# Kernel tuning notes

Measured on AMD Instinct MI355X. Metric: run time of the kernel, lower is better.

## Reference

```python
import jax, jax.numpy as jnp
import numpy as np

HIST_LEN = 100  # STDP history cap in the original module


def setup_inputs() -> dict:
    key = jax.random.key(0)
    ks = jax.random.split(key, 5)
    H, B = 1024, 16384
    return {
        "x": jax.random.normal(ks[0], (B, H), dtype=jnp.float32),
        "weights": jax.random.normal(ks[1], (H, H), dtype=jnp.float32) * 0.1,
        "meta_plasticity": jnp.ones((H,), dtype=jnp.float32),
        "pre_hist": jax.random.normal(ks[2], (HIST_LEN, H), dtype=jnp.float32) * 0.1,
        "post_hist": jax.random.normal(ks[3], (HIST_LEN, H), dtype=jnp.float32) * 0.1,
        "activity_history": jnp.zeros((1000,), dtype=jnp.float32),
        "history_pointer": 5,
        "stdp_window": jnp.float32(20.0),
        "stdp_decay": jnp.float32(0.1),
        "target_activity": jnp.float32(0.1),
        "homeostatic_rate": jnp.float32(0.01),
        "meta_learning_rate": jnp.float32(0.001),
    }


def reference(x, weights, meta_plasticity, pre_hist, post_hist,
              activity_history, history_pointer, stdp_window, stdp_decay,
              target_activity, homeostatic_rate, meta_learning_rate):
    # --- forward matmul: weights * meta_plasticity scales columns (broadcast over rows)
    output = x @ (weights * meta_plasticity)  # [B, H]

    # --- STDP update (vectorized form of the python loop over the history) ---
    # append current mean activities, pop oldest (steady-state length == HIST_LEN)
    pre = jnp.concatenate([pre_hist[1:], x.mean(axis=0)[None]], axis=0)       # [L, H]
    post = jnp.concatenate([post_hist[1:], output.mean(axis=0)[None]], axis=0)
    L = HIST_LEN
    i = jnp.arange(L, dtype=jnp.float32)
    dt = (L - i) * stdp_window
    w = 0.01 * jnp.exp(-dt * stdp_decay)                                      # [L]
    pos_w = jnp.where(i < L - 1, w, 0.0)   # i < len-1 branch
    neg_w = jnp.where(i > 0, w, 0.0)       # i > 0 branch
    # sum_i pos_w[i] * outer(post[-1], pre[i]) = outer(post[-1], pos_w @ pre)
    dW = jnp.outer(post[-1], pos_w @ pre) - jnp.outer(neg_w @ post, pre[-1])
    new_w = jnp.clip(weights + dW, -1.0, 1.0)

    # --- homeostatic plasticity ---
    hist = activity_history.at[history_pointer].set(output.mean())
    activity_diff = target_activity - hist.mean()
    new_w = jnp.clip(new_w * (1.0 + homeostatic_rate * activity_diff), -1.0, 1.0)

    # --- meta plasticity ---
    new_meta = jnp.clip(
        meta_plasticity + meta_learning_rate * (output.mean(axis=0) - meta_plasticity),
        0.0, 2.0)

    return output, new_w, new_meta, hist
```

## Files before the change

### kernel.cpp

```cpp
#include <hip/hip_runtime.h>
#include <hip/hip_bf16.h>

#define H 1024
#define BATCH 16384

typedef unsigned short u16;
typedef u16 u16x8 __attribute__((ext_vector_type(8)));
typedef __bf16 bf16x8 __attribute__((ext_vector_type(8)));
typedef float f32x4 __attribute__((ext_vector_type(4)));

typedef __attribute__((address_space(3))) unsigned int lds_uint;
typedef __attribute__((address_space(1))) const unsigned int glob_uint;

__device__ __forceinline__ u16 f2bf(float f) {
  unsigned int u = __float_as_uint(f);
  u += 0x7fffu + ((u >> 16) & 1u);
  return (u16)(u >> 16);
}

__global__ __launch_bounds__(256) void convx_kernel(const float* __restrict__ X,
                                                    u16* __restrict__ Xb,
                                                    float* __restrict__ xsum) {
  size_t r0 = (size_t)blockIdx.x * 64;
  int c = threadIdx.x;
  float s0 = 0.f, s1 = 0.f, s2 = 0.f, s3 = 0.f;
#pragma unroll 4
  for (int r = 0; r < 64; ++r) {
    size_t off = (r0 + r) * H + c * 4;
    const float4 v = *(const float4*)&X[off];
    ushort4 h;
    h.x = f2bf(v.x); h.y = f2bf(v.y); h.z = f2bf(v.z); h.w = f2bf(v.w);
    *(ushort4*)&Xb[off] = h;
    s0 += v.x; s1 += v.y; s2 += v.z; s3 += v.w;
  }
  atomicAdd(&xsum[c * 4 + 0], s0);
  atomicAdd(&xsum[c * 4 + 1], s1);
  atomicAdd(&xsum[c * 4 + 2], s2);
  atomicAdd(&xsum[c * 4 + 3], s3);
}

__global__ __launch_bounds__(256) void convw_kernel(const float* __restrict__ W,
                                                    u16* __restrict__ Wbt) {
  __shared__ __align__(16) u16 t[64][72];
  const int tid = threadIdx.x;
  const int n0 = blockIdx.x * 64, k0 = blockIdx.y * 64;
  const int rb = tid >> 4, c4 = tid & 15;
#pragma unroll
  for (int i = 0; i < 4; ++i) {
    int r = rb + i * 16;
    const float4 v = *(const float4*)&W[(size_t)(k0 + r) * H + n0 + c4 * 4];
    t[c4 * 4 + 0][r] = f2bf(v.x);
    t[c4 * 4 + 1][r] = f2bf(v.y);
    t[c4 * 4 + 2][r] = f2bf(v.z);
    t[c4 * 4 + 3][r] = f2bf(v.w);
  }
  __syncthreads();
  const int seg = tid & 7;
#pragma unroll
  for (int p = 0; p < 2; ++p) {
    int wr = p * 32 + (tid >> 3);
    *(u16x8*)&Wbt[(size_t)(n0 + wr) * H + k0 + seg * 8] = *(const u16x8*)&t[wr][seg * 8];
  }
}

__global__ __launch_bounds__(256) void gemm2_kernel(const u16* __restrict__ Xb,
                                                    const u16* __restrict__ Wbt,
                                                    const float* __restrict__ meta,
                                                    float* __restrict__ out) {
  __shared__ __align__(16) u16 lA[128 * 32];
  __shared__ __align__(16) u16 lB[128 * 32];

  const int tid = threadIdx.x;
  const int wave = tid >> 6;
  const int lane = tid & 63;
  const int quad = lane >> 4;
  const int l16 = lane & 15;
  const int wm = wave >> 1, wn = wave & 1;
  const size_t row0 = (size_t)blockIdx.x * 128;
  const int col0 = blockIdx.y * 128;

  const int sr = lane >> 2;
  const int sk = (lane & 3) * 8;

  f32x4 acc[4][4];
#pragma unroll
  for (int i = 0; i < 4; ++i)
#pragma unroll
    for (int j = 0; j < 4; ++j) acc[i][j] = (f32x4){0.f, 0.f, 0.f, 0.f};

  for (int k0 = 0; k0 < H; k0 += 32) {
#pragma unroll
    for (int i = 0; i < 2; ++i) {
      const int rg = i * 64 + wave * 16;
      const u16* ga = &Xb[(row0 + rg + sr) * H + k0 + sk];
      const u16* gb = &Wbt[(size_t)(col0 + rg + sr) * H + k0 + sk];
      __builtin_amdgcn_global_load_lds((glob_uint*)ga, (lds_uint*)&lA[rg * 32], 16, 0, 0);
      __builtin_amdgcn_global_load_lds((glob_uint*)gb, (lds_uint*)&lB[rg * 32], 16, 0, 0);
    }
    __syncthreads();

    bf16x8 av[4], bv[4];
#pragma unroll
    for (int f = 0; f < 4; ++f) {
      av[f] = __builtin_bit_cast(bf16x8, *(const u16x8*)&lA[(wm * 64 + f * 16 + l16) * 32 + quad * 8]);
      bv[f] = __builtin_bit_cast(bf16x8, *(const u16x8*)&lB[(wn * 64 + f * 16 + l16) * 32 + quad * 8]);
    }
#pragma unroll
    for (int fm = 0; fm < 4; ++fm)
#pragma unroll
      for (int fn = 0; fn < 4; ++fn)
        acc[fm][fn] = __builtin_amdgcn_mfma_f32_16x16x32_bf16(av[fm], bv[fn], acc[fm][fn], 0, 0, 0);
    __syncthreads();
  }

  float mcol[4];
#pragma unroll
  for (int fn = 0; fn < 4; ++fn) mcol[fn] = meta[col0 + wn * 64 + fn * 16 + l16];
#pragma unroll
  for (int fm = 0; fm < 4; ++fm) {
#pragma unroll
    for (int fn = 0; fn < 4; ++fn) {
      int col = col0 + wn * 64 + fn * 16 + l16;
#pragma unroll
      for (int r = 0; r < 4; ++r) {
        size_t row = row0 + wm * 64 + fm * 16 + quad * 4 + r;
        out[row * H + col] = acc[fm][fn][r] * mcol[fn];
      }
    }
  }
}

__global__ __launch_bounds__(256) void colsum_kernel(const float* __restrict__ x,
                                                     float* __restrict__ xsum) {
  int col = blockIdx.x * 256 + threadIdx.x;
  size_t r0 = (size_t)blockIdx.y * 256;
  float s = 0.f;
#pragma unroll 8
  for (int r = 0; r < 256; ++r) s += x[(r0 + r) * H + col];
  atomicAdd(&xsum[col], s);
}

__global__ __launch_bounds__(256) void gemm_fallback_kernel(const float* __restrict__ X,
                                                            const float* __restrict__ W,
                                                            const float* __restrict__ meta,
                                                            float* __restrict__ out) {
  __shared__ __align__(16) u16 lA[128][40];
  __shared__ __align__(16) u16 lB[128][40];
  const int tid = threadIdx.x;
  const int wave = tid >> 6;
  const int lane = tid & 63;
  const int quad = lane >> 4;
  const int l16 = lane & 15;
  const int wm = wave >> 1, wn = wave & 1;
  const size_t row0 = (size_t)blockIdx.x * 128;
  const int col0 = blockIdx.y * 128;
  f32x4 acc[4][4];
#pragma unroll
  for (int i = 0; i < 4; ++i)
#pragma unroll
    for (int j = 0; j < 4; ++j) acc[i][j] = (f32x4){0.f, 0.f, 0.f, 0.f};
  for (int k0 = 0; k0 < H; k0 += 32) {
#pragma unroll
    for (int i = 0; i < 4; ++i) {
      int idx = i * 256 + tid;
      int r = idx >> 3, c4 = idx & 7;
      const float4 v = *(const float4*)&X[(row0 + r) * H + k0 + c4 * 4];
      ushort4 h;
      h.x = f2bf(v.x); h.y = f2bf(v.y); h.z = f2bf(v.z); h.w = f2bf(v.w);
      *(ushort4*)&lA[r][c4 * 4] = h;
    }
#pragma unroll
    for (int i = 0; i < 4; ++i) {
      int idx = i * 256 + tid;
      int kk = idx >> 5, c4 = idx & 31;
      const float4 v = *(const float4*)&W[(size_t)(k0 + kk) * H + col0 + c4 * 4];
      lB[c4 * 4 + 0][kk] = f2bf(v.x);
      lB[c4 * 4 + 1][kk] = f2bf(v.y);
      lB[c4 * 4 + 2][kk] = f2bf(v.z);
      lB[c4 * 4 + 3][kk] = f2bf(v.w);
    }
    __syncthreads();
    bf16x8 av[4], bv[4];
#pragma unroll
    for (int f = 0; f < 4; ++f) {
      av[f] = __builtin_bit_cast(bf16x8, *(const u16x8*)&lA[wm * 64 + f * 16 + l16][quad * 8]);
      bv[f] = __builtin_bit_cast(bf16x8, *(const u16x8*)&lB[wn * 64 + f * 16 + l16][quad * 8]);
    }
#pragma unroll
    for (int fm = 0; fm < 4; ++fm)
#pragma unroll
      for (int fn = 0; fn < 4; ++fn)
        acc[fm][fn] = __builtin_amdgcn_mfma_f32_16x16x32_bf16(av[fm], bv[fn], acc[fm][fn], 0, 0, 0);
    __syncthreads();
  }
  float mcol[4];
#pragma unroll
  for (int fn = 0; fn < 4; ++fn) mcol[fn] = meta[col0 + wn * 64 + fn * 16 + l16];
#pragma unroll
  for (int fm = 0; fm < 4; ++fm) {
#pragma unroll
    for (int fn = 0; fn < 4; ++fn) {
      int col = col0 + wn * 64 + fn * 16 + l16;
#pragma unroll
      for (int r = 0; r < 4; ++r) {
        size_t row = row0 + wm * 64 + fm * 16 + quad * 4 + r;
        out[row * H + col] = acc[fm][fn][r] * mcol[fn];
      }
    }
  }
}

__global__ __launch_bounds__(256) void vecmat_kernel(const float* __restrict__ W,
                                                     const float* __restrict__ xsum,
                                                     float* __restrict__ outraw) {
  int j = blockIdx.x * 256 + threadIdx.x;
  int k0 = blockIdx.y * 64;
  float s = 0.f;
#pragma unroll 8
  for (int k = 0; k < 64; ++k) s += xsum[k0 + k] * W[(size_t)(k0 + k) * H + j];
  atomicAdd(&outraw[j], s * (1.0f / (float)BATCH));
}

__global__ __launch_bounds__(256) void stdpvec_kernel(const float* __restrict__ pre,
                                                      const float* __restrict__ post,
                                                      const float* __restrict__ win,
                                                      const float* __restrict__ dec,
                                                      float* __restrict__ posv,
                                                      float* __restrict__ negh) {
  int col = blockIdx.x * 256 + threadIdx.x;
  int t0 = 1 + blockIdx.y * 20;
  float wd = win[0] * dec[0];
  float ps = 0.f, ns = 0.f;
  int tend = t0 + 20;
  if (tend > 100) tend = 100;
  for (int t = t0; t < tend; ++t) {
    float w = 0.01f * expf(-(float)(101 - t) * wd);
    ps += w * pre[t * H + col];
    if (t >= 2) ns += w * post[t * H + col];
  }
  atomicAdd(&posv[col], ps);
  atomicAdd(&negh[col], ns);
}

__global__ __launch_bounds__(1024) void finalize_kernel(const float* __restrict__ meta,
                                                        const float* __restrict__ act,
                                                        const int* __restrict__ ptr,
                                                        const float* __restrict__ targ,
                                                        const float* __restrict__ homeo,
                                                        const float* __restrict__ mlr,
                                                        const float* __restrict__ outraw,
                                                        float* __restrict__ outmean,
                                                        float* __restrict__ scalep,
                                                        float* __restrict__ meta_out,
                                                        float* __restrict__ hist_out) {
  __shared__ float r1[16], r2[16];
  __shared__ float sc[2];
  int t = threadIdx.x;
  float om = meta[t] * outraw[t];
  outmean[t] = om;
  float a = (t < 1000) ? act[t] : 0.f;
  float s1 = om, s2 = a;
#pragma unroll
  for (int o = 32; o > 0; o >>= 1) {
    s1 += __shfl_down(s1, o, 64);
    s2 += __shfl_down(s2, o, 64);
  }
  if ((t & 63) == 0) { r1[t >> 6] = s1; r2[t >> 6] = s2; }
  __syncthreads();
  if (t == 0) {
    float ts1 = 0.f, ts2 = 0.f;
#pragma unroll
    for (int i = 0; i < 16; ++i) { ts1 += r1[i]; ts2 += r2[i]; }
    float total_mean = ts1 / (float)H;
    int p = ptr[0];
    float hist_mean = (ts2 - act[p] + total_mean) / 1000.f;
    float diff = targ[0] - hist_mean;
    sc[0] = 1.f + homeo[0] * diff;
    sc[1] = total_mean;
    scalep[0] = sc[0];
  }
  __syncthreads();
  float nm = meta[t] + mlr[0] * (om - meta[t]);
  nm = fminf(fmaxf(nm, 0.f), 2.f);
  meta_out[t] = nm;
  if (t < 1000) hist_out[t] = (t == ptr[0]) ? sc[1] : act[t];
}

__global__ __launch_bounds__(256) void neww_kernel(const float* __restrict__ W,
                                                   const float* __restrict__ outmean,
                                                   const float* __restrict__ posv,
                                                   const float* __restrict__ negh,
                                                   const float* __restrict__ xsum,
                                                   const float* __restrict__ scalep,
                                                   const float* __restrict__ win,
                                                   const float* __restrict__ dec,
                                                   float* __restrict__ out) {
  int idx = blockIdx.x * 256 + threadIdx.x;
  int rr = idx >> 10;
  int cc = idx & 1023;
  float w99 = 0.01f * expf(-win[0] * dec[0]);
  float scale = scalep[0];
  float om_r = outmean[rr];
  float neg_r = negh[rr] + w99 * om_r;
  float v = W[idx] + om_r * posv[cc] - neg_r * (xsum[cc] * (1.0f / (float)BATCH));
  v = fminf(fmaxf(v, -1.f), 1.f);
  v = v * scale;
  v = fminf(fmaxf(v, -1.f), 1.f);
  out[idx] = v;
}

extern "C" void kernel_launch(void* const* d_in, const int* in_sizes, int n_in,
                              void* d_out, int out_size, void* d_ws, size_t ws_size,
                              hipStream_t stream) {
  const float* x     = (const float*)d_in[0];
  const float* W     = (const float*)d_in[1];
  const float* meta  = (const float*)d_in[2];
  const float* pre   = (const float*)d_in[3];
  const float* post  = (const float*)d_in[4];
  const float* act   = (const float*)d_in[5];
  const int*   ptr   = (const int*)d_in[6];
  const float* win   = (const float*)d_in[7];
  const float* dec   = (const float*)d_in[8];
  const float* targ  = (const float*)d_in[9];
  const float* homeo = (const float*)d_in[10];
  const float* mlr   = (const float*)d_in[11];

  float* out_y    = (float*)d_out;
  float* out_w    = out_y + (size_t)BATCH * H;
  float* out_meta = out_w + (size_t)H * H;
  float* out_hist = out_meta + H;

  float* ws      = (float*)d_ws;
  float* xsum    = ws;
  float* outraw  = ws + 1024;
  float* outmean = ws + 2048;
  float* posv    = ws + 3072;
  float* negh    = ws + 4096;
  float* scalep  = ws + 5120;
  u16* Xb  = (u16*)(ws + 6144);
  u16* Wbt = Xb + (size_t)BATCH * H;

  const size_t ws_need = 6144 * sizeof(float) + ((size_t)BATCH * H + (size_t)H * H) * sizeof(u16);

  hipMemsetAsync(d_ws, 0, 6144 * sizeof(float), stream);

  if (ws_size >= ws_need) {
    convx_kernel<<<256, 256, 0, stream>>>(x, Xb, xsum);
    convw_kernel<<<dim3(16, 16), 256, 0, stream>>>(W, Wbt);
    gemm2_kernel<<<dim3(128, 8), 256, 0, stream>>>(Xb, Wbt, meta, out_y);
  } else {
    colsum_kernel<<<dim3(4, 64), 256, 0, stream>>>(x, xsum);
    gemm_fallback_kernel<<<dim3(128, 8), 256, 0, stream>>>(x, W, meta, out_y);
  }
  vecmat_kernel<<<dim3(4, 16), 256, 0, stream>>>(W, xsum, outraw);
  stdpvec_kernel<<<dim3(4, 5), 256, 0, stream>>>(pre, post, win, dec, posv, negh);
  finalize_kernel<<<1, 1024, 0, stream>>>(meta, act, ptr, targ, homeo, mlr,
                                          outraw, outmean, scalep, out_meta, out_hist);
  neww_kernel<<<4096, 256, 0, stream>>>(W, outmean, posv, negh, xsum, scalep, win, dec, out_w);
}
```

Measured before the change: 242.2 us.

## Merge prep, vecmat and STDP kernels; deepen GEMM K-tile; vectorize weight update

Merges the X conversion, W transpose-conversion and STDP vector partial sums into one launch that writes per-block partial column sums instead of using atomics, which removes the workspace memset. The vector-matrix product for output means now runs as extra blocks inside the GEMM launch. The GEMM K step doubles to 64 so each loop iteration has one barrier pair per 64 columns instead of per 32. The final weight update uses float4 loads and stores. Together this cuts launch count and serialization between small kernels, at the cost of a larger workspace and an extra reduction pass over the partial sums.

```diff
diff --git a/kernel.cpp b/kernel.cpp
--- a/kernel.cpp
+++ b/kernel.cpp
@@ -18,69 +18,121 @@
   return (u16)(u >> 16);
 }
 
-__global__ __launch_bounds__(256) void convx_kernel(const float* __restrict__ X,
-                                                    u16* __restrict__ Xb,
-                                                    float* __restrict__ xsum) {
-  size_t r0 = (size_t)blockIdx.x * 64;
-  int c = threadIdx.x;
-  float s0 = 0.f, s1 = 0.f, s2 = 0.f, s3 = 0.f;
+#define WS_XSUMP   0
+#define WS_XSUM    (WS_XSUMP + 256 * H)
+#define WS_ORAWP   (WS_XSUM + H)
+#define WS_POSVP   (WS_ORAWP + 16 * H)
+#define WS_NEGHP   (WS_POSVP + 5 * H)
+#define WS_OUTMEAN (WS_NEGHP + 5 * H)
+#define WS_POSV    (WS_OUTMEAN + H)
+#define WS_NEGH    (WS_POSV + H)
+#define WS_SCALEP  (WS_NEGH + H)
+#define WS_BF16    (WS_SCALEP + 16)
+
+__global__ __launch_bounds__(256) void prep_kernel(const float* __restrict__ X,
+                                                   const float* __restrict__ W,
+                                                   u16* __restrict__ Xb,
+                                                   u16* __restrict__ Wbt,
+                                                   float* __restrict__ ws,
+                                                   const float* __restrict__ pre,
+                                                   const float* __restrict__ post,
+                                                   const float* __restrict__ win,
+                                                   const float* __restrict__ dec) {
+  __shared__ __align__(16) u16 t[64][72];
+  const int b = blockIdx.x, tid = threadIdx.x;
+  if (b < 256) {
+    size_t r0 = (size_t)b * 64;
+    float s0 = 0.f, s1 = 0.f, s2 = 0.f, s3 = 0.f;
 #pragma unroll 4
-  for (int r = 0; r < 64; ++r) {
-    size_t off = (r0 + r) * H + c * 4;
-    const float4 v = *(const float4*)&X[off];
-    ushort4 h;
-    h.x = f2bf(v.x); h.y = f2bf(v.y); h.z = f2bf(v.z); h.w = f2bf(v.w);
-    *(ushort4*)&Xb[off] = h;
-    s0 += v.x; s1 += v.y; s2 += v.z; s3 += v.w;
-  }
-  atomicAdd(&xsum[c * 4 + 0], s0);
-  atomicAdd(&xsum[c * 4 + 1], s1);
-  atomicAdd(&xsum[c * 4 + 2], s2);
-  atomicAdd(&xsum[c * 4 + 3], s3);
-}
-
-__global__ __launch_bounds__(256) void convw_kernel(const float* __restrict__ W,
-                                                    u16* __restrict__ Wbt) {
-  __shared__ __align__(16) u16 t[64][72];
-  const int tid = threadIdx.x;
-  const int n0 = blockIdx.x * 64, k0 = blockIdx.y * 64;
-  const int rb = tid >> 4, c4 = tid & 15;
-#pragma unroll
-  for (int i = 0; i < 4; ++i) {
-    int r = rb + i * 16;
-    const float4 v = *(const float4*)&W[(size_t)(k0 + r) * H + n0 + c4 * 4];
-    t[c4 * 4 + 0][r] = f2bf(v.x);
-    t[c4 * 4 + 1][r] = f2bf(v.y);
-    t[c4 * 4 + 2][r] = f2bf(v.z);
-    t[c4 * 4 + 3][r] = f2bf(v.w);
-  }
-  __syncthreads();
-  const int seg = tid & 7;
-#pragma unroll
-  for (int p = 0; p < 2; ++p) {
-    int wr = p * 32 + (tid >> 3);
-    *(u16x8*)&Wbt[(size_t)(n0 + wr) * H + k0 + seg * 8] = *(const u16x8*)&t[wr][seg * 8];
-  }
-}
-
-__global__ __launch_bounds__(256) void gemm2_kernel(const u16* __restrict__ Xb,
-                                                    const u16* __restrict__ Wbt,
-                                                    const float* __restrict__ meta,
-                                                    float* __restrict__ out) {
-  __shared__ __align__(16) u16 lA[128 * 32];
-  __shared__ __align__(16) u16 lB[128 * 32];
-
-  const int tid = threadIdx.x;
+    for (int r = 0; r < 64; ++r) {
+      size_t off = (r0 + r) * H + tid * 4;
+      const float4 v = *(const float4*)&X[off];
+      ushort4 h;
+      h.x = f2bf(v.x); h.y = f2bf(v.y); h.z = f2bf(v.z); h.w = f2bf(v.w);
+      *(ushort4*)&Xb[off] = h;
+      s0 += v.x; s1 += v.y; s2 += v.z; s3 += v.w;
+    }
+    float* row = &ws[WS_XSUMP + b * H];
+    row[tid * 4 + 0] = s0; row[tid * 4 + 1] = s1;
+    row[tid * 4 + 2] = s2; row[tid * 4 + 3] = s3;
+  } else if (b < 512) {
+    const int b2 = b - 256;
+    const int n0 = (b2 & 15) * 64, k0 = (b2 >> 4) * 64;
+    const int rb = tid >> 4, c4 = tid & 15;
+#pragma unroll
+    for (int i = 0; i < 4; ++i) {
+      int r = rb + i * 16;
+      const float4 v = *(const float4*)&W[(size_t)(k0 + r) * H + n0 + c4 * 4];
+      t[c4 * 4 + 0][r] = f2bf(v.x);
+      t[c4 * 4 + 1][r] = f2bf(v.y);
+      t[c4 * 4 + 2][r] = f2bf(v.z);
+      t[c4 * 4 + 3][r] = f2bf(v.w);
+    }
+    __syncthreads();
+    const int seg = tid & 7;
+#pragma unroll
+    for (int p = 0; p < 2; ++p) {
+      int wr = p * 32 + (tid >> 3);
+      *(u16x8*)&Wbt[(size_t)(n0 + wr) * H + k0 + seg * 8] = *(const u16x8*)&t[wr][seg * 8];
+    }
+  } else {
+    const int b2 = b - 512;
+    const int col = (b2 & 3) * 256 + tid;
+    const int seg = b2 >> 2;
+    const int t0 = 1 + seg * 20;
+    int tend = t0 + 20; if (tend > 100) tend = 100;
+    float wd = win[0] * dec[0];
+    float ps = 0.f, ns = 0.f;
+    for (int tt = t0; tt < tend; ++tt) {
+      float w = 0.01f * expf(-(float)(101 - tt) * wd);
+      ps += w * pre[tt * H + col];
+      if (tt >= 2) ns += w * post[tt * H + col];
+    }
+    ws[WS_POSVP + seg * H + col] = ps;
+    ws[WS_NEGHP + seg * H + col] = ns;
+  }
+}
+
+__global__ __launch_bounds__(256) void gemm_vm_kernel(const u16* __restrict__ Xb,
+                                                      const u16* __restrict__ Wbt,
+                                                      const float* __restrict__ meta,
+                                                      const float* __restrict__ W,
+                                                      float* __restrict__ ws,
+                                                      float* __restrict__ out) {
+  __shared__ __align__(16) u16 lA[8192];
+  __shared__ __align__(16) u16 lB[8192];
+  __shared__ float xs[64];
+
+  const int b = blockIdx.x, tid = threadIdx.x;
+
+  if (b < 64) {
+    const int jx = b & 3, ky = b >> 2;
+    if (tid < 64) {
+      float s = 0.f;
+      const float* p = &ws[WS_XSUMP + ky * 64 + tid];
+#pragma unroll 8
+      for (int q = 0; q < 256; ++q) s += p[q * H];
+      xs[tid] = s;
+      if (jx == 0) ws[WS_XSUM + ky * 64 + tid] = s;
+    }
+    __syncthreads();
+    const int j = jx * 256 + tid;
+    float s = 0.f;
+#pragma unroll 8
+    for (int k = 0; k < 64; ++k) s += xs[k] * W[(size_t)(ky * 64 + k) * H + j];
+    ws[WS_ORAWP + ky * H + j] = s * (1.0f / (float)BATCH);
+    return;
+  }
+
+  const int bg = b - 64;
+  const int mt = bg & 127, nt = bg >> 7;
+  const size_t row0 = (size_t)mt * 128;
+  const int col0 = nt * 128;
   const int wave = tid >> 6;
   const int lane = tid & 63;
   const int quad = lane >> 4;
   const int l16 = lane & 15;
   const int wm = wave >> 1, wn = wave & 1;
-  const size_t row0 = (size_t)blockIdx.x * 128;
-  const int col0 = blockIdx.y * 128;
-
-  const int sr = lane >> 2;
-  const int sk = (lane & 3) * 8;
 
   f32x4 acc[4][4];
 #pragma unroll
@@ -88,28 +140,37 @@
 #pragma unroll
     for (int j = 0; j < 4; ++j) acc[i][j] = (f32x4){0.f, 0.f, 0.f, 0.f};
 
-  for (int k0 = 0; k0 < H; k0 += 32) {
-#pragma unroll
-    for (int i = 0; i < 2; ++i) {
-      const int rg = i * 64 + wave * 16;
-      const u16* ga = &Xb[(row0 + rg + sr) * H + k0 + sk];
-      const u16* gb = &Wbt[(size_t)(col0 + rg + sr) * H + k0 + sk];
-      __builtin_amdgcn_global_load_lds((glob_uint*)ga, (lds_uint*)&lA[rg * 32], 16, 0, 0);
-      __builtin_amdgcn_global_load_lds((glob_uint*)gb, (lds_uint*)&lB[rg * 32], 16, 0, 0);
-    }
-    __syncthreads();
-
-    bf16x8 av[4], bv[4];
-#pragma unroll
-    for (int f = 0; f < 4; ++f) {
-      av[f] = __builtin_bit_cast(bf16x8, *(const u16x8*)&lA[(wm * 64 + f * 16 + l16) * 32 + quad * 8]);
-      bv[f] = __builtin_bit_cast(bf16x8, *(const u16x8*)&lB[(wn * 64 + f * 16 + l16) * 32 + quad * 8]);
-    }
-#pragma unroll
-    for (int fm = 0; fm < 4; ++fm)
-#pragma unroll
-      for (int fn = 0; fn < 4; ++fn)
-        acc[fm][fn] = __builtin_amdgcn_mfma_f32_16x16x32_bf16(av[fm], bv[fn], acc[fm][fn], 0, 0, 0);
+  for (int k0 = 0; k0 < H; k0 += 64) {
+#pragma unroll
+    for (int i = 0; i < 4; ++i) {
+      const int c = wave * 4 + i;
+      const int half = c >> 3;
+      const int rr = (c & 7) * 16 + (lane >> 2);
+      const int kk = half * 32 + (lane & 3) * 8;
+      const u16* ga = &Xb[(row0 + rr) * H + k0 + kk];
+      const u16* gb = &Wbt[(size_t)(col0 + rr) * H + k0 + kk];
+      u16* la = &lA[half * 4096 + (c & 7) * 512];
+      u16* lb = &lB[half * 4096 + (c & 7) * 512];
+      __builtin_amdgcn_global_load_lds((glob_uint*)ga, (lds_uint*)la, 16, 0, 0);
+      __builtin_amdgcn_global_load_lds((glob_uint*)gb, (lds_uint*)lb, 16, 0, 0);
+    }
+    __syncthreads();
+#pragma unroll
+    for (int ks = 0; ks < 2; ++ks) {
+      bf16x8 av[4], bv[4];
+#pragma unroll
+      for (int f = 0; f < 4; ++f) {
+        av[f] = __builtin_bit_cast(bf16x8,
+            *(const u16x8*)&lA[ks * 4096 + (wm * 64 + f * 16 + l16) * 32 + quad * 8]);
+        bv[f] = __builtin_bit_cast(bf16x8,
+            *(const u16x8*)&lB[ks * 4096 + (wn * 64 + f * 16 + l16) * 32 + quad * 8]);
+      }
+#pragma unroll
+      for (int fm = 0; fm < 4; ++fm)
+#pragma unroll
+        for (int fn = 0; fn < 4; ++fn)
+          acc[fm][fn] = __builtin_amdgcn_mfma_f32_16x16x32_bf16(av[fm], bv[fn], acc[fm][fn], 0, 0, 0);
+    }
     __syncthreads();
   }
 
@@ -128,6 +189,92 @@
       }
     }
   }
+}
+
+__global__ __launch_bounds__(1024) void finalize2_kernel(const float* __restrict__ meta,
+                                                         const float* __restrict__ act,
+                                                         const int* __restrict__ ptr,
+                                                         const float* __restrict__ targ,
+                                                         const float* __restrict__ homeo,
+                                                         const float* __restrict__ mlr,
+                                                         float* __restrict__ ws,
+                                                         float* __restrict__ meta_out,
+                                                         float* __restrict__ hist_out) {
+  __shared__ float r1[16], r2[16];
+  __shared__ float sc[2];
+  int t = threadIdx.x;
+  float oraw = 0.f;
+#pragma unroll
+  for (int i = 0; i < 16; ++i) oraw += ws[WS_ORAWP + i * H + t];
+  float om = meta[t] * oraw;
+  ws[WS_OUTMEAN + t] = om;
+  float pv = 0.f, nv = 0.f;
+#pragma unroll
+  for (int i = 0; i < 5; ++i) { pv += ws[WS_POSVP + i * H + t]; nv += ws[WS_NEGHP + i * H + t]; }
+  ws[WS_POSV + t] = pv;
+  ws[WS_NEGH + t] = nv;
+
+  float a = (t < 1000) ? act[t] : 0.f;
+  float s1 = om, s2 = a;
+#pragma unroll
+  for (int o = 32; o > 0; o >>= 1) {
+    s1 += __shfl_down(s1, o, 64);
+    s2 += __shfl_down(s2, o, 64);
+  }
+  if ((t & 63) == 0) { r1[t >> 6] = s1; r2[t >> 6] = s2; }
+  __syncthreads();
+  if (t == 0) {
+    float ts1 = 0.f, ts2 = 0.f;
+#pragma unroll
+    for (int i = 0; i < 16; ++i) { ts1 += r1[i]; ts2 += r2[i]; }
+    float total_mean = ts1 / (float)H;
+    int p = ptr[0];
+    float hist_mean = (ts2 - act[p] + total_mean) / 1000.f;
+    float diff = targ[0] - hist_mean;
+    sc[0] = 1.f + homeo[0] * diff;
+    sc[1] = total_mean;
+    ws[WS_SCALEP] = sc[0];
+  }
+  __syncthreads();
+  float nm = meta[t] + mlr[0] * (om - meta[t]);
+  nm = fminf(fmaxf(nm, 0.f), 2.f);
+  meta_out[t] = nm;
+  if (t < 1000) hist_out[t] = (t == ptr[0]) ? sc[1] : act[t];
+}
+
+__global__ __launch_bounds__(256) void neww_kernel(const float* __restrict__ W,
+                                                   const float* __restrict__ outmean,
+                                                   const float* __restrict__ posv,
+                                                   const float* __restrict__ negh,
+                                                   const float* __restrict__ xsum,
+                                                   const float* __restrict__ scalep,
+                                                   const float* __restrict__ win,
+                                                   const float* __restrict__ dec,
+                                                   float* __restrict__ out) {
+  int idx4 = blockIdx.x * 256 + threadIdx.x;
+  int rr = idx4 >> 8;
+  int c4 = (idx4 & 255) * 4;
+  float w99 = 0.01f * expf(-win[0] * dec[0]);
+  float scale = scalep[0];
+  float om_r = outmean[rr];
+  float neg_r = negh[rr] + w99 * om_r;
+  const float4 wv = *(const float4*)&W[(size_t)rr * H + c4];
+  const float4 pv = *(const float4*)&posv[c4];
+  const float4 xv = *(const float4*)&xsum[c4];
+  float4 o;
+  float vx[4] = {wv.x, wv.y, wv.z, wv.w};
+  float px[4] = {pv.x, pv.y, pv.z, pv.w};
+  float xx[4] = {xv.x, xv.y, xv.z, xv.w};
+  float ox[4];
+#pragma unroll
+  for (int i = 0; i < 4; ++i) {
+    float v = vx[i] + om_r * px[i] - neg_r * (xx[i] * (1.0f / (float)BATCH));
+    v = fminf(fmaxf(v, -1.f), 1.f);
+    v = v * scale;
+    ox[i] = fminf(fmaxf(v, -1.f), 1.f);
+  }
+  o.x = ox[0]; o.y = ox[1]; o.z = ox[2]; o.w = ox[3];
+  *(float4*)&out[(size_t)rr * H + c4] = o;
 }
 
 __global__ __launch_bounds__(256) void colsum_kernel(const float* __restrict__ x,
@@ -286,29 +433,6 @@
   if (t < 1000) hist_out[t] = (t == ptr[0]) ? sc[1] : act[t];
 }
 
-__global__ __launch_bounds__(256) void neww_kernel(const float* __restrict__ W,
-                                                   const float* __restrict__ outmean,
-                                                   const float* __restrict__ posv,
-                                                   const float* __restrict__ negh,
-                                                   const float* __restrict__ xsum,
-                                                   const float* __restrict__ scalep,
-                                                   const float* __restrict__ win,
-                                                   const float* __restrict__ dec,
-                                                   float* __restrict__ out) {
-  int idx = blockIdx.x * 256 + threadIdx.x;
-  int rr = idx >> 10;
-  int cc = idx & 1023;
-  float w99 = 0.01f * expf(-win[0] * dec[0]);
-  float scale = scalep[0];
-  float om_r = outmean[rr];
-  float neg_r = negh[rr] + w99 * om_r;
-  float v = W[idx] + om_r * posv[cc] - neg_r * (xsum[cc] * (1.0f / (float)BATCH));
-  v = fminf(fmaxf(v, -1.f), 1.f);
-  v = v * scale;
-  v = fminf(fmaxf(v, -1.f), 1.f);
-  out[idx] = v;
-}
-
 extern "C" void kernel_launch(void* const* d_in, const int* in_sizes, int n_in,
                               void* d_out, int out_size, void* d_ws, size_t ws_size,
                               hipStream_t stream) {
@@ -330,31 +454,34 @@
   float* out_meta = out_w + (size_t)H * H;
   float* out_hist = out_meta + H;
 
-  float* ws      = (float*)d_ws;
-  float* xsum    = ws;
-  float* outraw  = ws + 1024;
-  float* outmean = ws + 2048;
-  float* posv    = ws + 3072;
-  float* negh    = ws + 4096;
-  float* scalep  = ws + 5120;
-  u16* Xb  = (u16*)(ws + 6144);
+  float* ws = (float*)d_ws;
+  u16* Xb  = (u16*)(ws + WS_BF16);
   u16* Wbt = Xb + (size_t)BATCH * H;
 
-  const size_t ws_need = 6144 * sizeof(float) + ((size_t)BATCH * H + (size_t)H * H) * sizeof(u16);
-
-  hipMemsetAsync(d_ws, 0, 6144 * sizeof(float), stream);
+  const size_t ws_need = (size_t)WS_BF16 * sizeof(float) +
+                         ((size_t)BATCH * H + (size_t)H * H) * sizeof(u16);
 
   if (ws_size >= ws_need) {
-    convx_kernel<<<256, 256, 0, stream>>>(x, Xb, xsum);
-    convw_kernel<<<dim3(16, 16), 256, 0, stream>>>(W, Wbt);
-    gemm2_kernel<<<dim3(128, 8), 256, 0, stream>>>(Xb, Wbt, meta, out_y);
+    prep_kernel<<<532, 256, 0, stream>>>(x, W, Xb, Wbt, ws, pre, post, win, dec);
+    gemm_vm_kernel<<<1088, 256, 0, stream>>>(Xb, Wbt, meta, W, ws, out_y);
+    finalize2_kernel<<<1, 1024, 0, stream>>>(meta, act, ptr, targ, homeo, mlr,
+                                             ws, out_meta, out_hist);
+    neww_kernel<<<1024, 256, 0, stream>>>(W, ws + WS_OUTMEAN, ws + WS_POSV, ws + WS_NEGH,
+                                          ws + WS_XSUM, ws + WS_SCALEP, win, dec, out_w);
   } else {
+    float* xsum    = ws;
+    float* outraw  = ws + 1024;
+    float* outmean = ws + 2048;
+    float* posv    = ws + 3072;
+    float* negh    = ws + 4096;
+    float* scalep  = ws + 5120;
+    hipMemsetAsync(d_ws, 0, 6144 * sizeof(float), stream);
     colsum_kernel<<<dim3(4, 64), 256, 0, stream>>>(x, xsum);
     gemm_fallback_kernel<<<dim3(128, 8), 256, 0, stream>>>(x, W, meta, out_y);
-  }
-  vecmat_kernel<<<dim3(4, 16), 256, 0, stream>>>(W, xsum, outraw);
-  stdpvec_kernel<<<dim3(4, 5), 256, 0, stream>>>(pre, post, win, dec, posv, negh);
-  finalize_kernel<<<1, 1024, 0, stream>>>(meta, act, ptr, targ, homeo, mlr,
-                                          outraw, outmean, scalep, out_meta, out_hist);
-  neww_kernel<<<4096, 256, 0, stream>>>(W, outmean, posv, negh, xsum, scalep, win, dec, out_w);
-}
+    vecmat_kernel<<<dim3(4, 16), 256, 0, stream>>>(W, xsum, outraw);
+    stdpvec_kernel<<<dim3(4, 5), 256, 0, stream>>>(pre, post, win, dec, posv, negh);
+    finalize_kernel<<<1, 1024, 0, stream>>>(meta, act, ptr, targ, homeo, mlr,
+                                            outraw, outmean, scalep, out_meta, out_hist);
+    neww_kernel<<<1024, 256, 0, stream>>>(W, outmean, posv, negh, xsum, scalep, win, dec, out_w);
+  }
+}
```

Result: faster. 224.7 us (-7.2%).
